# Kernel tuning notes

Hardware: AMD Instinct MI355X
Metric: run time of the kernel (lower is better)

## Reference

```python
import jax, jax.numpy as jnp
import numpy as np

XY_SCALE = 10.0
N_HEAD = 4
B, N, M, L, E, FA = 2, 64, 64, 30, 128, 16


def rel_xysc(x1, x2):
    # x = [x, y, sin(h), cos(h)]; pose of x2 expressed in x1's frame
    dx = x2[..., 0] - x1[..., 0]
    dy = x2[..., 1] - x1[..., 1]
    s1, c1 = x1[..., 2], x1[..., 3]
    s2, c2 = x2[..., 2], x2[..., 3]
    rx = c1 * dx + s1 * dy
    ry = -s1 * dx + c1 * dy
    rs = s2 * c1 - c2 * s1
    rc = c2 * c1 + s2 * s1
    return jnp.stack([rx, ry, rs, rc], -1)


def _linear_params(k, din, dout):
    kw, kb = jax.random.split(k)
    w = jax.random.normal(kw, (din, dout), jnp.float32) / np.sqrt(din)
    b = jax.random.normal(kb, (dout,), jnp.float32) * 0.01
    return w, b


def setup_inputs():
    key = jax.random.key(0)
    ks = jax.random.split(key, 10)
    agent = jax.random.normal(ks[0], (B, N, FA), jnp.float32)
    lane = jax.random.normal(ks[1], (B, M, 4 * L), jnp.float32)
    We, be = _linear_params(ks[2], 4, E)            # edge_embed_net
    Wa, ba = _linear_params(ks[3], FA - 4, E)        # agent_embed_net (agent_feat_dim=12)
    pe = jax.random.normal(ks[4], (L, E), jnp.float32)
    Wq, bq = _linear_params(ks[5], E, E)
    Wk, bk = _linear_params(ks[6], E, E)
    Wv, bv = _linear_params(ks[7], E, E)
    Wo, bo = _linear_params(ks[8], E, E)
    Wp, bp = _linear_params(ks[9], E, E)             # proj (output_dim=E)
    return {"agent": agent, "lane": lane, "We": We, "be": be, "Wa": Wa, "ba": ba,
            "pe": pe, "Wq": Wq, "bq": bq, "Wk": Wk, "bk": bk, "Wv": Wv, "bv": bv,
            "Wo": Wo, "bo": bo, "Wp": Wp, "bp": bp}


def reference(agent, lane, We, be, Wa, ba, pe, Wq, bq, Wk, bk, Wv, bv, Wo, bo, Wp, bp):
    b, n, fa = agent.shape
    m = lane.shape[1]
    l = lane.shape[2] // 4
    e = pe.shape[1]
    h, dh = N_HEAD, e // N_HEAD

    ax = agent[..., jnp.array([0, 1, 3, 4])]                      # (B,N,4) xysc
    afeat = jnp.concatenate([agent[..., 2:3], agent[..., 5:]], -1)  # (B,N,12)
    lp = lane.reshape(b, m * l, 4)                                # lane points

    # relative pose of every lane point in every agent frame: (B,N,M*L,4)
    rel = rel_xysc(ax[:, :, None, :], lp[:, None, :, :])
    rel = jnp.concatenate([rel[..., :2] / XY_SCALE, rel[..., 2:]], -1)
    f1 = jnp.logical_not(jnp.all(ax == 0, -1)).astype(agent.dtype)  # (B,N)
    f2 = jnp.logical_not(jnp.all(lp == 0, -1)).astype(agent.dtype)  # (B,M*L)
    rel = rel * f1[:, :, None, None] * f2[:, None, :, None]
    edge = rel.reshape(b, n, m, l, 4)

    # edge embedding + positional embedding
    ee = edge @ We + be + pe[:l][None, None, None]                 # (B,N,M,L,E)
    ae = afeat @ Wa + ba                                           # (B,N,E)

    # cross-attention: single query (agent) over L lane points, per (b,n,m)
    q = (ae @ Wq + bq).reshape(b, n, h, dh)                        # (B,N,H,dh)
    k = (ee @ Wk + bk).reshape(b, n, m, l, h, dh)
    v = (ee @ Wv + bv).reshape(b, n, m, l, h, dh)
    scores = jnp.einsum('bnhd,bnmlhd->bnmhl', q, k) / np.sqrt(dh).astype(np.float32)
    w = jax.nn.softmax(scores, axis=-1)
    attn = jnp.einsum('bnmhl,bnmlhd->bnmhd', w, v).reshape(b, n, m, e)
    attn = attn @ Wo + bo                                          # attention out proj
    return attn @ Wp + bp                                          # (B,N,M,E)
```

## Files before the change

kernel.cpp:

```cpp
#include <hip/hip_runtime.h>
#include <hip/hip_bf16.h>

#define L_ 30
#define NB 2
#define NN 64
#define NM 64
#define MCH 16

#define O_WOP  0
#define O_CVP  16384
#define O_WEWV 20224
#define O_WAWQ 20736
#define O_BQQ  22272
#define O_CK   22400
#define O_WEWK 26240
#define O_BOP  26752
#define O_QS   26880
#define O_GT   43264

typedef __attribute__((ext_vector_type(8))) short short8;
typedef __attribute__((ext_vector_type(4))) float f32x4;

__device__ __forceinline__ unsigned short f2b(float v) {
    union { float f; unsigned int u; } x; x.f = v;
    unsigned int u = x.u + 0x7FFFu + ((x.u >> 16) & 1u);
    return (unsigned short)(u >> 16);
}
__device__ __forceinline__ float dot4(float4 a, float4 b) {
    return a.x*b.x + a.y*b.y + a.z*b.z + a.w*b.w;
}

__global__ __launch_bounds__(256)
void kA(const float* __restrict__ We,  const float* __restrict__ be,
        const float* __restrict__ Wa,  const float* __restrict__ ba,
        const float* __restrict__ pe,
        const float* __restrict__ Wq,  const float* __restrict__ bq,
        const float* __restrict__ Wk,  const float* __restrict__ bk,
        const float* __restrict__ Wv,  const float* __restrict__ bv,
        const float* __restrict__ Wo,  const float* __restrict__ bo,
        const float* __restrict__ Wp,  const float* __restrict__ bp,
        float* __restrict__ ws) {
    const int t = threadIdx.x;
    const int b = blockIdx.x;
    const int e = t & 127;
    const int rr = t >> 7;

    if (b < 64) {
        const int d = 2*b + rr;
        const float* wo = Wo + d*128;
        float acc = 0.f;
        #pragma unroll 32
        for (int x = 0; x < 128; ++x) acc += wo[x] * Wp[x*128 + e];
        ws[O_WOP + d*128 + e] = acc;
    } else if (b < 79) {
        const int l = 2*(b-64) + rr;
        const float* pl = pe + l*128;
        float acc = bv[e];
        #pragma unroll 32
        for (int d = 0; d < 128; ++d) acc += (be[d] + pl[d]) * Wv[d*128 + e];
        ws[O_CVP + l*128 + e] = acc;
    } else if (b < 94) {
        const int l = 2*(b-79) + rr;
        const float* pl = pe + l*128;
        float acc = bk[e];
        #pragma unroll 32
        for (int d = 0; d < 128; ++d) acc += (be[d] + pl[d]) * Wk[d*128 + e];
        ws[O_CK + l*128 + e] = acc;
    } else if (b < 96) {
        const int j = 2*(b-94) + rr;
        const float* wj = We + j*128;
        float acc = 0.f;
        #pragma unroll 32
        for (int d = 0; d < 128; ++d) acc += wj[d] * Wv[d*128 + e];
        ws[O_WEWV + j*128 + e] = acc;
    } else if (b < 98) {
        const int j = 2*(b-96) + rr;
        const float* wj = We + j*128;
        float acc = 0.f;
        #pragma unroll 32
        for (int d = 0; d < 128; ++d) acc += wj[d] * Wk[d*128 + e];
        ws[O_WEWK + j*128 + e] = acc;
    } else if (b < 104) {
        const int f = 2*(b-98) + rr;
        const float* wf = Wa + f*128;
        float acc = 0.f;
        #pragma unroll 32
        for (int d = 0; d < 128; ++d) acc += wf[d] * Wq[d*128 + e];
        ws[O_WAWQ + f*128 + e] = acc;
    } else {
        if (rr == 0) {
            float acc = bq[e];
            #pragma unroll 32
            for (int d = 0; d < 128; ++d) acc += ba[d] * Wq[d*128 + e];
            ws[O_BQQ + e] = acc;
        } else {
            float acc = bp[e];
            #pragma unroll 32
            for (int d = 0; d < 128; ++d) acc += bo[d] * Wp[d*128 + e];
            ws[O_BOP + e] = acc;
        }
    }
}

__global__ __launch_bounds__(256)
void kB(const float* __restrict__ agent, float* __restrict__ ws) {
    const int t = threadIdx.x;
    const int b = blockIdx.x;
    const int e = t & 127;
    const int rr = t >> 7;
    unsigned short* GT = (unsigned short*)(ws + O_GT);

    if (b < 68) {
        const int k = 2*b + rr;
        const float* scal;
        int h;
        if (k < 16) { h = k >> 2; scal = ws + O_WEWV + (k & 3)*128 + h*32; }
        else { int r = k - 16; h = r / 30; int l = r - h*30;
               scal = ws + O_CVP + l*128 + h*32; }
        const float* wop = ws + O_WOP + (h*32)*128 + e;
        float acc = 0.f;
        #pragma unroll
        for (int c = 0; c < 32; ++c) acc += scal[c] * wop[c*128];
        GT[e*168 + k] = f2b(acc);
    } else if (b < 132) {
        const int r = 2*(b-68) + rr;
        const float* ag = agent + r*16;
        const float* wq = ws + O_WAWQ;
        float acc = ws[O_BQQ + e];
        acc += ag[2] * wq[e];
        #pragma unroll
        for (int f = 1; f < 12; ++f) acc += ag[4+f] * wq[f*128 + e];
        ws[O_QS + r*128 + e] = acc * 0.17677669529663687f;
    } else {
        for (int idx = t; idx < 32*128; idx += 256) {
            int row = 136 + (idx >> 7);
            GT[(idx & 127)*168 + row] = 0;
        }
    }
}

__global__ __launch_bounds__(256)
void k_main(const float* __restrict__ agent, const float* __restrict__ lane,
            const float* __restrict__ ws, float* __restrict__ out) {

    __shared__ __align__(16) float ScE[16][124];
    __shared__ __align__(16) unsigned short WcB[16][168];
    __shared__ __align__(16) float uc_s[136];

    const int t = threadIdx.x;
    const int bid = blockIdx.x;
    const int bn = bid >> 2;
    const int m0 = (bid & 3) * MCH;
    const int b = bn >> 6;

    const unsigned short* GT = (const unsigned short*)(ws + O_GT);
    const int lane_id = t & 63;
    const int wv = t >> 6;
    const int frm = lane_id & 15;
    const int kg  = lane_id >> 4;
    const int e0 = wv*32 + frm;
    short8 g0[5], g1[5];
    #pragma unroll
    for (int i = 0; i < 5; ++i) {
        g0[i] = *(const short8*)&GT[(size_t)e0*168 + i*32 + kg*8];
        g1[i] = *(const short8*)&GT[(size_t)(e0+16)*168 + i*32 + kg*8];
    }
    const float bb0 = ws[O_BOP + e0];
    const float bb1 = ws[O_BOP + e0 + 16];

    for (int i = t; i < 16*24; i += 256) {
        int m = i / 24;
        WcB[m][136 + (i - m*24)] = 0;
    }
    if (t < 136) {
        if (t < 16) {
            int h = t >> 2, j = t & 3;
            const float4* x = (const float4*)(ws + O_WEWK + j*128 + h*32);
            const float4* y = (const float4*)(ws + O_QS + bn*128 + h*32);
            float a = 0.f;
            #pragma unroll
            for (int i = 0; i < 8; ++i) a += dot4(x[i], y[i]);
            uc_s[t] = a;
        } else {
            int r = t - 16; int h = r/30, l = r - h*30;
            const float4* x = (const float4*)(ws + O_CK + l*128 + h*32);
            const float4* y = (const float4*)(ws + O_QS + bn*128 + h*32);
            float a = 0.f;
            #pragma unroll
            for (int i = 0; i < 8; ++i) a += dot4(x[i], y[i]);
            uc_s[t] = a;
        }
    }
    const float ax  = agent[bn*16+0], ay = agent[bn*16+1];
    const float as_ = agent[bn*16+3], ac = agent[bn*16+4];
    const float f1 = (ax==0.f && ay==0.f && as_==0.f && ac==0.f) ? 0.f : 1.f;
    for (int job = t; job < MCH*30; job += 256) {
        int m = job / 30, l = job - m*30;
        const float* lp = lane + (size_t)((b*NM + m0 + m)*L_ + l)*4;
        float4 lv = *(const float4*)lp;
        float f2 = (lv.x==0.f && lv.y==0.f && lv.z==0.f && lv.w==0.f) ? 0.f : 1.f;
        float f = f1 * f2;
        float dx = lv.x - ax, dy = lv.y - ay;
        float4 ev;
        ev.x = (ac*dx + as_*dy) * 0.1f * f;
        ev.y = (ac*dy - as_*dx) * 0.1f * f;
        ev.z = (lv.z*ac - lv.w*as_) * f;
        ev.w = (lv.w*ac + lv.z*as_) * f;
        *(float4*)&ScE[m][l*4] = ev;
    }
    __syncthreads();

    {
        const int m = t >> 4, hh = (t >> 2) & 3, s = t & 3;
        float4 u4 = *(const float4*)&uc_s[hh*4];
        float4 e4[8];
        float sc[8];
        float mx = -1e30f;
        #pragma unroll
        for (int k = 0; k < 8; ++k) {
            int l = s + 4*k;
            if (l < 30) {
                e4[k] = *(const float4*)&ScE[m][l*4];
                sc[k] = e4[k].x*u4.x + e4[k].y*u4.y + e4[k].z*u4.z + e4[k].w*u4.w
                      + uc_s[16 + hh*30 + l];
            } else {
                e4[k] = make_float4(0.f,0.f,0.f,0.f);
                sc[k] = -1e30f;
            }
            mx = fmaxf(mx, sc[k]);
        }
        mx = fmaxf(mx, __shfl_xor(mx, 1, 64));
        mx = fmaxf(mx, __shfl_xor(mx, 2, 64));
        float sum = 0.f;
        float wvv[8];
        #pragma unroll
        for (int k = 0; k < 8; ++k) {
            float evv = __expf(sc[k] - mx);
            evv = (s + 4*k < 30) ? evv : 0.f;
            wvv[k] = evv; sum += evv;
        }
        sum += __shfl_xor(sum, 1, 64);
        sum += __shfl_xor(sum, 2, 64);
        const float inv = 1.f / sum;
        float4 p = make_float4(0.f,0.f,0.f,0.f);
        #pragma unroll
        for (int k = 0; k < 8; ++k) {
            int l = s + 4*k;
            if (l < 30) {
                float w = wvv[k] * inv;
                WcB[m][16 + hh*30 + l] = f2b(w);
                p.x += w * e4[k].x; p.y += w * e4[k].y;
                p.z += w * e4[k].z; p.w += w * e4[k].w;
            }
        }
        p.x += __shfl_xor(p.x, 1, 64); p.y += __shfl_xor(p.y, 1, 64);
        p.z += __shfl_xor(p.z, 1, 64); p.w += __shfl_xor(p.w, 1, 64);
        p.x += __shfl_xor(p.x, 2, 64); p.y += __shfl_xor(p.y, 2, 64);
        p.z += __shfl_xor(p.z, 2, 64); p.w += __shfl_xor(p.w, 2, 64);
        float mine = (s == 0) ? p.x : (s == 1) ? p.y : (s == 2) ? p.z : p.w;
        WcB[m][hh*4 + s] = f2b(mine);
    }
    __syncthreads();

    {
        f32x4 acc0 = {bb0, bb0, bb0, bb0};
        f32x4 acc1 = {bb1, bb1, bb1, bb1};
        #pragma unroll
        for (int i = 0; i < 5; ++i) {
            short8 a = *(const short8*)&WcB[frm][i*32 + kg*8];
            acc0 = __builtin_amdgcn_mfma_f32_16x16x32_bf16(a, g0[i], acc0, 0, 0, 0);
            acc1 = __builtin_amdgcn_mfma_f32_16x16x32_bf16(a, g1[i], acc1, 0, 0, 0);
        }
        float* ob = out + ((size_t)(bn*NM + m0))*128;
        #pragma unroll
        for (int r = 0; r < 4; ++r) {
            int m = kg*4 + r;
            ob[m*128 + e0]      = acc0[r];
            ob[m*128 + e0 + 16] = acc1[r];
        }
    }
}

extern "C" void kernel_launch(void* const* d_in, const int* in_sizes, int n_in,
                              void* d_out, int out_size, void* d_ws, size_t ws_size,
                              hipStream_t stream) {
    const float* agent = (const float*)d_in[0];
    const float* lane  = (const float*)d_in[1];
    const float* We = (const float*)d_in[2];
    const float* be = (const float*)d_in[3];
    const float* Wa = (const float*)d_in[4];
    const float* ba = (const float*)d_in[5];
    const float* pe = (const float*)d_in[6];
    const float* Wq = (const float*)d_in[7];
    const float* bq = (const float*)d_in[8];
    const float* Wk = (const float*)d_in[9];
    const float* bk = (const float*)d_in[10];
    const float* Wv = (const float*)d_in[11];
    const float* bv = (const float*)d_in[12];
    const float* Wo = (const float*)d_in[13];
    const float* bo = (const float*)d_in[14];
    const float* Wp = (const float*)d_in[15];
    const float* bp = (const float*)d_in[16];
    float* ws  = (float*)d_ws;
    float* out = (float*)d_out;

    hipLaunchKernelGGL(kA, dim3(105), dim3(256), 0, stream,
                       We, be, Wa, ba, pe, Wq, bq, Wk, bk, Wv, bv, Wo, bo, Wp, bp, ws);
    hipLaunchKernelGGL(kB, dim3(133), dim3(256), 0, stream, agent, ws);
    hipLaunchKernelGGL(k_main, dim3(NB*NN*4), dim3(256), 0, stream,
                       agent, lane, ws, out);
}
```

Baseline: 19.91 us.

## Drop the folding kernel and apply Wo·Wp as a second MFMA stage in main kernel

Removes the intermediate kernel kB that folded the per-head value weights into Wo·Wp and computed query vectors. kA now writes a block-diagonal bf16 value matrix and a transposed bf16 Wo·Wp directly. The main kernel computes the query per agent in shared memory and runs two chained MFMA stages through a shared bf16 buffer. This saves one kernel launch and its dependency. In exchange it adds per-block MFMA work, an extra barrier, redundant query computation across blocks, and an additional bf16 rounding of the intermediate.

```diff
diff --git a/kernel.cpp b/kernel.cpp
--- a/kernel.cpp
+++ b/kernel.cpp
@@ -7,16 +7,13 @@
 #define NM 64
 #define MCH 16
 
-#define O_WOP  0
-#define O_CVP  16384
-#define O_WEWV 20224
-#define O_WAWQ 20736
-#define O_BQQ  22272
-#define O_CK   22400
-#define O_WEWK 26240
-#define O_BOP  26752
-#define O_QS   26880
-#define O_GT   43264
+#define O_WAWQ 0
+#define O_BQQ  1536
+#define O_CK   1664
+#define O_WEWK 5504
+#define O_BOP  6016
+#define O_SCT  6144
+#define O_WOPT 16896
 
 typedef __attribute__((ext_vector_type(8))) short short8;
 typedef __attribute__((ext_vector_type(4))) float f32x4;
@@ -44,6 +41,8 @@
     const int b = blockIdx.x;
     const int e = t & 127;
     const int rr = t >> 7;
+    unsigned short* SCT  = (unsigned short*)(ws + O_SCT);
+    unsigned short* WOPT = (unsigned short*)(ws + O_WOPT);
 
     if (b < 64) {
         const int d = 2*b + rr;
@@ -51,28 +50,36 @@
         float acc = 0.f;
         #pragma unroll 32
         for (int x = 0; x < 128; ++x) acc += wo[x] * Wp[x*128 + e];
-        ws[O_WOP + d*128 + e] = acc;
+        WOPT[e*128 + d] = f2b(acc);
     } else if (b < 79) {
         const int l = 2*(b-64) + rr;
+        const int h = e >> 5;
         const float* pl = pe + l*128;
         float acc = bv[e];
         #pragma unroll 32
         for (int d = 0; d < 128; ++d) acc += (be[d] + pl[d]) * Wv[d*128 + e];
-        ws[O_CVP + l*128 + e] = acc;
-    } else if (b < 94) {
-        const int l = 2*(b-79) + rr;
+        unsigned short v = f2b(acc);
+        #pragma unroll
+        for (int hh = 0; hh < 4; ++hh)
+            SCT[e*168 + 16 + hh*30 + l] = (hh == h) ? v : (unsigned short)0;
+    } else if (b < 81) {
+        const int j = 2*(b-79) + rr;
+        const int h = e >> 5;
+        const float* wj = We + j*128;
+        float acc = 0.f;
+        #pragma unroll 32
+        for (int d = 0; d < 128; ++d) acc += wj[d] * Wv[d*128 + e];
+        unsigned short v = f2b(acc);
+        #pragma unroll
+        for (int hh = 0; hh < 4; ++hh)
+            SCT[e*168 + hh*4 + j] = (hh == h) ? v : (unsigned short)0;
+    } else if (b < 96) {
+        const int l = 2*(b-81) + rr;
         const float* pl = pe + l*128;
         float acc = bk[e];
         #pragma unroll 32
         for (int d = 0; d < 128; ++d) acc += (be[d] + pl[d]) * Wk[d*128 + e];
         ws[O_CK + l*128 + e] = acc;
-    } else if (b < 96) {
-        const int j = 2*(b-94) + rr;
-        const float* wj = We + j*128;
-        float acc = 0.f;
-        #pragma unroll 32
-        for (int d = 0; d < 128; ++d) acc += wj[d] * Wv[d*128 + e];
-        ws[O_WEWV + j*128 + e] = acc;
     } else if (b < 98) {
         const int j = 2*(b-96) + rr;
         const float* wj = We + j*128;
@@ -87,7 +94,7 @@
         #pragma unroll 32
         for (int d = 0; d < 128; ++d) acc += wf[d] * Wq[d*128 + e];
         ws[O_WAWQ + f*128 + e] = acc;
-    } else {
+    } else if (b == 104) {
         if (rr == 0) {
             float acc = bq[e];
             #pragma unroll 32
@@ -99,42 +106,10 @@
             for (int d = 0; d < 128; ++d) acc += bo[d] * Wp[d*128 + e];
             ws[O_BOP + e] = acc;
         }
-    }
-}
-
-__global__ __launch_bounds__(256)
-void kB(const float* __restrict__ agent, float* __restrict__ ws) {
-    const int t = threadIdx.x;
-    const int b = blockIdx.x;
-    const int e = t & 127;
-    const int rr = t >> 7;
-    unsigned short* GT = (unsigned short*)(ws + O_GT);
-
-    if (b < 68) {
-        const int k = 2*b + rr;
-        const float* scal;
-        int h;
-        if (k < 16) { h = k >> 2; scal = ws + O_WEWV + (k & 3)*128 + h*32; }
-        else { int r = k - 16; h = r / 30; int l = r - h*30;
-               scal = ws + O_CVP + l*128 + h*32; }
-        const float* wop = ws + O_WOP + (h*32)*128 + e;
-        float acc = 0.f;
-        #pragma unroll
-        for (int c = 0; c < 32; ++c) acc += scal[c] * wop[c*128];
-        GT[e*168 + k] = f2b(acc);
-    } else if (b < 132) {
-        const int r = 2*(b-68) + rr;
-        const float* ag = agent + r*16;
-        const float* wq = ws + O_WAWQ;
-        float acc = ws[O_BQQ + e];
-        acc += ag[2] * wq[e];
-        #pragma unroll
-        for (int f = 1; f < 12; ++f) acc += ag[4+f] * wq[f*128 + e];
-        ws[O_QS + r*128 + e] = acc * 0.17677669529663687f;
     } else {
-        for (int idx = t; idx < 32*128; idx += 256) {
-            int row = 136 + (idx >> 7);
-            GT[(idx & 127)*168 + row] = 0;
+        for (int i = t; i < 128*32; i += 256) {
+            int c = i >> 5, k = 136 + (i & 31);
+            SCT[c*168 + k] = 0;
         }
     }
 }
@@ -145,7 +120,9 @@
 
     __shared__ __align__(16) float ScE[16][124];
     __shared__ __align__(16) unsigned short WcB[16][168];
+    __shared__ __align__(16) unsigned short T_s[16][136];
     __shared__ __align__(16) float uc_s[136];
+    __shared__ __align__(16) float qs_s[128];
 
     const int t = threadIdx.x;
     const int bid = blockIdx.x;
@@ -153,43 +130,39 @@
     const int m0 = (bid & 3) * MCH;
     const int b = bn >> 6;
 
-    const unsigned short* GT = (const unsigned short*)(ws + O_GT);
+    const unsigned short* SCT  = (const unsigned short*)(ws + O_SCT);
+    const unsigned short* WOPT = (const unsigned short*)(ws + O_WOPT);
     const int lane_id = t & 63;
     const int wv = t >> 6;
     const int frm = lane_id & 15;
     const int kg  = lane_id >> 4;
     const int e0 = wv*32 + frm;
-    short8 g0[5], g1[5];
+    short8 s0[5], s1[5];
     #pragma unroll
     for (int i = 0; i < 5; ++i) {
-        g0[i] = *(const short8*)&GT[(size_t)e0*168 + i*32 + kg*8];
-        g1[i] = *(const short8*)&GT[(size_t)(e0+16)*168 + i*32 + kg*8];
+        s0[i] = *(const short8*)&SCT[e0*168 + i*32 + kg*8];
+        s1[i] = *(const short8*)&SCT[(e0+16)*168 + i*32 + kg*8];
+    }
+    short8 w0[4], w1[4];
+    #pragma unroll
+    for (int i = 0; i < 4; ++i) {
+        w0[i] = *(const short8*)&WOPT[e0*128 + i*32 + kg*8];
+        w1[i] = *(const short8*)&WOPT[(e0+16)*128 + i*32 + kg*8];
     }
     const float bb0 = ws[O_BOP + e0];
     const float bb1 = ws[O_BOP + e0 + 16];
 
-    for (int i = t; i < 16*24; i += 256) {
-        int m = i / 24;
-        WcB[m][136 + (i - m*24)] = 0;
-    }
-    if (t < 136) {
-        if (t < 16) {
-            int h = t >> 2, j = t & 3;
-            const float4* x = (const float4*)(ws + O_WEWK + j*128 + h*32);
-            const float4* y = (const float4*)(ws + O_QS + bn*128 + h*32);
-            float a = 0.f;
-            #pragma unroll
-            for (int i = 0; i < 8; ++i) a += dot4(x[i], y[i]);
-            uc_s[t] = a;
-        } else {
-            int r = t - 16; int h = r/30, l = r - h*30;
-            const float4* x = (const float4*)(ws + O_CK + l*128 + h*32);
-            const float4* y = (const float4*)(ws + O_QS + bn*128 + h*32);
-            float a = 0.f;
-            #pragma unroll
-            for (int i = 0; i < 8; ++i) a += dot4(x[i], y[i]);
-            uc_s[t] = a;
-        }
+    if (t < 128) {
+        const float* ag = agent + bn*16;
+        float acc = ws[O_BQQ + t];
+        acc += ag[2] * ws[O_WAWQ + t];
+        #pragma unroll
+        for (int f = 1; f < 12; ++f) acc += ag[4+f] * ws[O_WAWQ + f*128 + t];
+        qs_s[t] = acc * 0.17677669529663687f;
+    }
+    for (int i = t; i < 16*32; i += 256) {
+        int m = i >> 5;
+        WcB[m][136 + (i & 31)] = 0;
     }
     const float ax  = agent[bn*16+0], ay = agent[bn*16+1];
     const float as_ = agent[bn*16+3], ac = agent[bn*16+4];
@@ -210,6 +183,25 @@
     }
     __syncthreads();
 
+    if (t < 136) {
+        float a = 0.f;
+        if (t < 16) {
+            int h = t >> 2, j = t & 3;
+            const float4* x = (const float4*)(ws + O_WEWK + j*128 + h*32);
+            const float4* y = (const float4*)&qs_s[h*32];
+            #pragma unroll
+            for (int i = 0; i < 8; ++i) a += dot4(x[i], y[i]);
+        } else {
+            int r = t - 16; int h = r/30, l = r - h*30;
+            const float4* x = (const float4*)(ws + O_CK + l*128 + h*32);
+            const float4* y = (const float4*)&qs_s[h*32];
+            #pragma unroll
+            for (int i = 0; i < 8; ++i) a += dot4(x[i], y[i]);
+        }
+        uc_s[t] = a;
+    }
+    __syncthreads();
+
     {
         const int m = t >> 4, hh = (t >> 2) & 3, s = t & 3;
         float4 u4 = *(const float4*)&uc_s[hh*4];
@@ -263,13 +255,30 @@
     __syncthreads();
 
     {
+        f32x4 a0 = {0.f,0.f,0.f,0.f};
+        f32x4 a1 = {0.f,0.f,0.f,0.f};
+        #pragma unroll
+        for (int i = 0; i < 5; ++i) {
+            short8 a = *(const short8*)&WcB[frm][i*32 + kg*8];
+            a0 = __builtin_amdgcn_mfma_f32_16x16x32_bf16(a, s0[i], a0, 0, 0, 0);
+            a1 = __builtin_amdgcn_mfma_f32_16x16x32_bf16(a, s1[i], a1, 0, 0, 0);
+        }
+        #pragma unroll
+        for (int r = 0; r < 4; ++r) {
+            T_s[kg*4 + r][e0]      = f2b(a0[r]);
+            T_s[kg*4 + r][e0 + 16] = f2b(a1[r]);
+        }
+    }
+    __syncthreads();
+
+    {
         f32x4 acc0 = {bb0, bb0, bb0, bb0};
         f32x4 acc1 = {bb1, bb1, bb1, bb1};
         #pragma unroll
-        for (int i = 0; i < 5; ++i) {
-            short8 a = *(const short8*)&WcB[frm][i*32 + kg*8];
-            acc0 = __builtin_amdgcn_mfma_f32_16x16x32_bf16(a, g0[i], acc0, 0, 0, 0);
-            acc1 = __builtin_amdgcn_mfma_f32_16x16x32_bf16(a, g1[i], acc1, 0, 0, 0);
+        for (int i = 0; i < 4; ++i) {
+            short8 a2 = *(const short8*)&T_s[frm][i*32 + kg*8];
+            acc0 = __builtin_amdgcn_mfma_f32_16x16x32_bf16(a2, w0[i], acc0, 0, 0, 0);
+            acc1 = __builtin_amdgcn_mfma_f32_16x16x32_bf16(a2, w1[i], acc1, 0, 0, 0);
         }
         float* ob = out + ((size_t)(bn*NM + m0))*128;
         #pragma unroll
@@ -304,9 +313,8 @@
     float* ws  = (float*)d_ws;
     float* out = (float*)d_out;
 
-    hipLaunchKernelGGL(kA, dim3(105), dim3(256), 0, stream,
+    hipLaunchKernelGGL(kA, dim3(106), dim3(256), 0, stream,
                        We, be, Wa, ba, pe, Wq, bq, Wk, bk, Wv, bv, Wo, bo, Wp, bp, ws);
-    hipLaunchKernelGGL(kB, dim3(133), dim3(256), 0, stream, agent, ws);
     hipLaunchKernelGGL(k_main, dim3(NB*NN*4), dim3(256), 0, stream,
                        agent, lane, ws, out);
 }
```

After: 18.14 us. -8.9%, faster.
